# Kernel optimization log

Hardware: AMD Instinct MI355X
Metric: run time of the kernel (lower is better)

Reference implementation:

```python
import jax, jax.numpy as jnp
import numpy as np

NUM_HEADS = 16

def setup_inputs() -> dict:
    key = jax.random.key(0)
    ks = jax.random.split(key, 6)
    B, S, D = 2, 2048, 1024
    scale = 1.0 / np.sqrt(D)
    x = jax.random.normal(ks[0], (B, S, D), dtype=jnp.float32)
    mask = jnp.tril(jnp.ones((S, S), dtype=jnp.int32))[None, None, :, :]  # causal [1,1,S,S]
    Wq = jax.random.normal(ks[1], (D, D), dtype=jnp.float32) * scale
    Wk = jax.random.normal(ks[2], (D, D), dtype=jnp.float32) * scale
    Wv = jax.random.normal(ks[3], (D, D), dtype=jnp.float32) * scale
    Wo = jax.random.normal(ks[4], (D, D), dtype=jnp.float32) * scale
    z = jnp.zeros((D,), dtype=jnp.float32)
    return {"x": x, "mask": mask, "Wq": Wq, "bq": z, "Wk": Wk, "bk": z,
            "Wv": Wv, "bv": z, "Wo": Wo, "bo": z}

def reference(x, mask, Wq, bq, Wk, bk, Wv, bv, Wo, bo):
    B, S, D = x.shape
    H = NUM_HEADS
    hd = D // H
    # torch Linear: y = x @ W.T + b
    def proj(W, b):
        return (x @ W.T + b).reshape(B, S, H, hd).transpose(0, 2, 1, 3)  # [B,H,S,hd]
    q = proj(Wq, bq)
    k = proj(Wk, bk)
    v = proj(Wv, bv)
    # NOTE: original module does NOT scale by 1/sqrt(d_k) -- faithful to source.
    scores = jnp.einsum('bhqd,bhkd->bhqk', q, k)  # [B,H,S,S]
    scores = jnp.where(mask == 0, jnp.float32(-10000.0), scores)
    attn = jax.nn.softmax(scores, axis=-1)
    # dropout omitted for deterministic reference (eval-mode equivalent)
    out = jnp.einsum('bhqk,bhkd->bhqd', attn, v)
    out = out.transpose(0, 2, 1, 3).reshape(B, S, D)
    return out @ Wo.T + bo
```

## Files before the change

### kernel.cpp

```cpp
#include <hip/hip_runtime.h>

#define S_LEN 2048
#define DM    1024
#define NHEAD 16
#define HDIM  64
#define NB    2
#define NROWS (NB * S_LEN)
#define RCP_LN2 1.44269504f

using f32x4  = __attribute__((ext_vector_type(4))) float;
using f16x8  = __attribute__((ext_vector_type(8))) _Float16;
using f16x2  = __attribute__((ext_vector_type(2))) _Float16;

__device__ __forceinline__ ushort f2h(float f) {
  return __builtin_bit_cast(ushort, (_Float16)f);
}
__device__ __forceinline__ unsigned pkrtz(float a, float b) {
  return __builtin_bit_cast(unsigned, __builtin_amdgcn_cvt_pkrtz(a, b));
}
__device__ __forceinline__ f32x4 mfma16(f16x8 a, f16x8 b, f32x4 c) {
  return __builtin_amdgcn_mfma_f32_16x16x32_f16(a, b, c, 0, 0, 0);
}
__device__ __forceinline__ void async16(const ushort* g, ushort* l) {
  __builtin_amdgcn_global_load_lds(
      (const __attribute__((address_space(1))) unsigned*)g,
      (__attribute__((address_space(3))) unsigned*)l, 16, 0, 0);
}

__global__ void tohalf5(const float* __restrict__ x,  const float* __restrict__ wq,
                        const float* __restrict__ wk, const float* __restrict__ wv,
                        const float* __restrict__ wo,
                        ushort* __restrict__ Xh, ushort* __restrict__ Wh,
                        ushort* __restrict__ Woh) {
  constexpr int X4 = (NROWS * DM) / 4;
  constexpr int W4 = (DM * DM) / 4;
  const size_t WN = (size_t)DM * DM;
  int i = blockIdx.x * 256 + threadIdx.x;
  const float4* src; ushort4* dst; int k;
  if (i < X4)               { src = (const float4*)x;  dst = (ushort4*)Xh;        k = i; }
  else if (i < X4 + W4)     { src = (const float4*)wq; dst = (ushort4*)Wh;        k = i - X4; }
  else if (i < X4 + 2*W4)   { src = (const float4*)wk; dst = (ushort4*)(Wh+WN);   k = i - X4 - W4; }
  else if (i < X4 + 3*W4)   { src = (const float4*)wv; dst = (ushort4*)(Wh+2*WN); k = i - X4 - 2*W4; }
  else                      { src = (const float4*)wo; dst = (ushort4*)Woh;       k = i - X4 - 3*W4; }
  float4 v = src[k];
  dst[k] = make_ushort4(f2h(v.x), f2h(v.y), f2h(v.z), f2h(v.w));
}

template<int EPI, int MFRAG, int NFRAG>
__global__ __launch_bounds__(256, 4)
void gemm_half(const ushort* __restrict__ A, const ushort* __restrict__ B,
               const float* __restrict__ biasQ, const float* __restrict__ biasK,
               const float* __restrict__ biasV,
               float* __restrict__ outF,
               ushort* __restrict__ Q, ushort* __restrict__ Kd,
               ushort* __restrict__ Vt, int Ncols)
{
  constexpr int KD = 1024;
  constexpr int BM = MFRAG * 32, BN = NFRAG * 32;
  constexpr int NCH = (BM + BN) / 8;
  constexpr int CPW = NCH / 4;
  __shared__ ushort sL[(BM + BN) * 64];
  const int t = threadIdx.x;
  const int w = t >> 6, l = t & 63;
  const int lr = l >> 4, lc = l & 15;
  const int wr = w >> 1, wc = w & 1;
  const int nwg = gridDim.x * gridDim.y;
  const int lin = blockIdx.y * gridDim.x + blockIdx.x;
  const int per8 = nwg >> 3;
  const int swz = (lin & 7) * per8 + (lin >> 3);
  const int i0 = (swz / gridDim.x) * BM, j0 = (swz % gridDim.x) * BN;

  const int srow = l >> 3;
  const int se   = ((l & 7) ^ srow) << 3;

  f32x4 acc[MFRAG][NFRAG] = {};

  for (int k0 = 0; k0 < KD; k0 += 64) {
#pragma unroll
    for (int ii = 0; ii < CPW; ++ii) {
      const int c = w * CPW + ii;
      const ushort* src = (c < BM / 8)
          ? A + (size_t)(i0 + c * 8 + srow) * KD + k0 + se
          : B + (size_t)(j0 + (c - BM / 8) * 8 + srow) * KD + k0 + se;
      async16(src, &sL[c * 512]);
    }
    asm volatile("s_waitcnt vmcnt(0)" ::: "memory");
    __syncthreads();
#pragma unroll
    for (int kk = 0; kk < 2; ++kk) {
      const int cb = (kk * 64 + lr * 16) ^ ((lc & 7) << 4);
      f16x8 a[MFRAG], b[NFRAG];
#pragma unroll
      for (int m = 0; m < MFRAG; ++m)
        a[m] = *(const f16x8*)&sL[(wr * MFRAG * 16 + m * 16 + lc) * 64 + (cb >> 1)];
#pragma unroll
      for (int n = 0; n < NFRAG; ++n)
        b[n] = *(const f16x8*)&sL[BM * 64 + (wc * NFRAG * 16 + n * 16 + lc) * 64 + (cb >> 1)];
#pragma unroll
      for (int m = 0; m < MFRAG; ++m)
#pragma unroll
        for (int n = 0; n < NFRAG; ++n)
          acc[m][n] = mfma16(a[m], b[n], acc[m][n]);
    }
    __syncthreads();
  }

#pragma unroll
  for (int m = 0; m < MFRAG; ++m)
#pragma unroll
    for (int n = 0; n < NFRAG; ++n) {
      const int jbase = j0 + wc * NFRAG * 16 + n * 16;
      const int ibase = i0 + wr * MFRAG * 16 + m * 16 + lr * 4;
      if constexpr (EPI == 0) {
        const int region = jbase >> 10;
        const int jc0 = jbase & 1023;
        const int h = jc0 >> 6, d0 = jc0 & 63;
        const int b = ibase >> 11, s0 = ibase & 2047;
        const size_t bh = (size_t)(b * NHEAD + h);
        if (region == 0) {
          float bb = biasQ[jc0 + lc];
#pragma unroll
          for (int r = 0; r < 4; ++r)
            Q[(bh * S_LEN + s0 + r) * HDIM + d0 + lc] =
                f2h((acc[m][n][r] + bb) * RCP_LN2);
        } else if (region == 1) {
          float bb = biasK[jc0 + lc];
#pragma unroll
          for (int r = 0; r < 4; ++r)
            Kd[(bh * S_LEN + s0 + r) * HDIM + d0 + lc] = f2h(acc[m][n][r] + bb);
        } else {
          float bb = biasV[jc0 + lc];
          ushort4 pv = make_ushort4(f2h(acc[m][n][0] + bb), f2h(acc[m][n][1] + bb),
                                    f2h(acc[m][n][2] + bb), f2h(acc[m][n][3] + bb));
          *(ushort4*)&Vt[(bh * HDIM + d0 + lc) * S_LEN + s0] = pv;
        }
      } else {
#pragma unroll
        for (int r = 0; r < 4; ++r)
          outF[(size_t)(ibase + r) * Ncols + jbase + lc] =
              acc[m][n][r] + biasQ[jbase + lc];
      }
    }
}

__global__ __launch_bounds__(128, 4)
void attn_kernel(const ushort* __restrict__ Qp, const ushort* __restrict__ Kp,
                 const ushort* __restrict__ Vt, ushort* __restrict__ O)
{
  __shared__ ushort sKV[2 * 64 * 64];
  __shared__ ushort Plds[2][16][72];
  const int lin = blockIdx.x;
  const int v  = 63 - (lin >> 5);
  const int bh = lin & 31;
  const int t = threadIdx.x, w = t >> 6, l = t & 63;
  const int g = l >> 4, q = l & 15;
  const size_t base = (size_t)bh * S_LEN * HDIM;
  const int q0 = v * 32 + w * 16;
  const int nkt = (v >> 1) + 1;

  const int srow = l >> 3;
  const int se   = ((l & 7) ^ srow) << 3;

  f16x8 bQ[2];
#pragma unroll
  for (int ks = 0; ks < 2; ++ks)
    bQ[ks] = *(const f16x8*)(Qp + base + (size_t)(q0 + q) * HDIM + ks * 32 + g * 8);

  f32x4 oacc[4] = {};
  float m = -3e38f, lsum = 0.f;

  for (int kt = 0; kt < nkt; ++kt) {
#pragma unroll
    for (int ii = 0; ii < 8; ++ii) {
      const int c = w * 8 + ii;
      const int sel = c >> 3, sub = c & 7;
      const ushort* src =
          sel == 0 ? Kp + base + (size_t)(kt * 64 + sub * 8 + srow) * HDIM + se
                   : Vt + ((size_t)bh * HDIM + sub * 8 + srow) * S_LEN + kt * 64 + se;
      async16(src, &sKV[sel * 4096 + sub * 512]);
    }
    asm volatile("s_waitcnt vmcnt(0)" ::: "memory");
    __syncthreads();

    f32x4 s[4] = {};
#pragma unroll
    for (int ks = 0; ks < 2; ++ks) {
      const int cb = (((ks * 64 + g * 16) ^ ((q & 7) << 4)) >> 1);
#pragma unroll
      for (int n = 0; n < 4; ++n) {
        f16x8 kf = *(const f16x8*)&sKV[(n * 16 + q) * 64 + cb];
        s[n] = mfma16(kf, bQ[ks], s[n]);
      }
    }
    if (kt == nkt - 1) {
      const int qg = q0 + q;
#pragma unroll
      for (int n = 0; n < 4; ++n)
#pragma unroll
        for (int r = 0; r < 4; ++r) {
          int kg = kt * 64 + n * 16 + g * 4 + r;
          if (kg > qg) s[n][r] = -1e30f;
        }
    }
    float pm = -3e38f;
#pragma unroll
    for (int n = 0; n < 4; ++n) {
      pm = fmaxf(pm, fmaxf(fmaxf(s[n][0], s[n][1]), fmaxf(s[n][2], s[n][3])));
    }
    pm = fmaxf(pm, __shfl_xor(pm, 16));
    pm = fmaxf(pm, __shfl_xor(pm, 32));
    if (__any(pm > m + 8.0f)) {
      float mnew = fmaxf(m, pm);
      float sc = exp2f(m - mnew);
      m = mnew;
      float scr[4];
#pragma unroll
      for (int r = 0; r < 4; ++r) scr[r] = __shfl(sc, g * 4 + r);
#pragma unroll
      for (int dt = 0; dt < 4; ++dt)
#pragma unroll
        for (int r = 0; r < 4; ++r) oacc[dt][r] *= scr[r];
      lsum *= sc;
    }
    float rs = 0.f;
#pragma unroll
    for (int n = 0; n < 4; ++n)
#pragma unroll
      for (int r = 0; r < 4; ++r) {
        float pe = exp2f(s[n][r] - m);
        s[n][r] = pe;
        rs += pe;
      }
    rs += __shfl_xor(rs, 16);
    rs += __shfl_xor(rs, 32);
    lsum += rs;

#pragma unroll
    for (int n = 0; n < 4; ++n) {
      uint2 pk = make_uint2(pkrtz(s[n][0], s[n][1]), pkrtz(s[n][2], s[n][3]));
      *(uint2*)&Plds[w][q][n * 16 + g * 4] = pk;
    }
#pragma unroll
    for (int ks = 0; ks < 2; ++ks) {
      f16x8 ap = *(const f16x8*)&Plds[w][q][ks * 32 + g * 8];
      const int cb = (((ks * 64 + g * 16) ^ ((q & 7) << 4)) >> 1);
#pragma unroll
      for (int dt = 0; dt < 4; ++dt) {
        f16x8 bv = *(const f16x8*)&sKV[4096 + (dt * 16 + q) * 64 + cb];
        oacc[dt] = mfma16(ap, bv, oacc[dt]);
      }
    }
    __syncthreads();
  }

  float lsr[4];
#pragma unroll
  for (int r = 0; r < 4; ++r)
    lsr[r] = __builtin_amdgcn_rcpf(__shfl(lsum, g * 4 + r));
  const int b = bh >> 4, h = bh & 15;
#pragma unroll
  for (int dt = 0; dt < 4; ++dt)
#pragma unroll
    for (int r = 0; r < 4; ++r) {
      int qg = q0 + g * 4 + r;
      O[((size_t)b * S_LEN + qg) * DM + h * HDIM + dt * 16 + q] =
          f2h(oacc[dt][r] * lsr[r]);
    }
}

extern "C" void kernel_launch(void* const* d_in, const int* in_sizes, int n_in,
                              void* d_out, int out_size, void* d_ws, size_t ws_size,
                              hipStream_t stream)
{
  const float* x  = (const float*)d_in[0];
  const float* Wq = (const float*)d_in[2];
  const float* bq = (const float*)d_in[3];
  const float* Wk = (const float*)d_in[4];
  const float* bk = (const float*)d_in[5];
  const float* Wv = (const float*)d_in[6];
  const float* bv = (const float*)d_in[7];
  const float* Wo = (const float*)d_in[8];
  const float* bo = (const float*)d_in[9];
  float* out = (float*)d_out;

  char* ws = (char*)d_ws;
  size_t off = 0;
  auto alloc = [&](size_t bytes) { char* p = ws + off; off += bytes; return p; };
  const size_t XN = (size_t)NROWS * DM;
  const size_t WN = (size_t)DM * DM;

  ushort* Xh  = (ushort*)alloc(XN * 2);
  ushort* Wh  = (ushort*)alloc(3 * WN * 2);
  ushort* Woh = (ushort*)alloc(WN * 2);
  ushort* Qb  = (ushort*)alloc(XN * 2);
  ushort* Kb  = (ushort*)alloc(XN * 2);
  ushort* Vt  = (ushort*)alloc(XN * 2);
  ushort* Ob  = (ushort*)alloc(XN * 2);
  (void)ws_size; (void)in_sizes; (void)n_in; (void)out_size;

  const int total4 = (int)(XN / 4 + 4 * (WN / 4));
  tohalf5<<<total4 / 256, 256, 0, stream>>>(x, Wq, Wk, Wv, Wo, Xh, Wh, Woh);

  gemm_half<0, 4, 4><<<dim3(24, 32), 256, 0, stream>>>(
      Xh, Wh, bq, bk, bv, nullptr, Qb, Kb, Vt, 3072);
  attn_kernel<<<2048, 128, 0, stream>>>(Qb, Kb, Vt, Ob);
  gemm_half<1, 2, 4><<<dim3(8, 64), 256, 0, stream>>>(
      Ob, Woh, bo, nullptr, nullptr, out, nullptr, nullptr, nullptr, 1024);
}
```

Measured before the change: 122.6 us.

## Enlarge attention query tile to 128 rows with double-buffered K/V staging

Each attention block now covers 128 query rows with 4 waves, each wave handling two 16-row sub-tiles, so every K/V tile loaded into LDS is reused by twice as many queries. K/V loads are double-buffered so the next tile is fetched while the current one is computed, and waves skip tiles that lie fully above their causal diagonal. This reduces global K/V traffic and exposed load latency, at the cost of more registers and LDS per block, fewer blocks (512), and possible load imbalance between waves in the causal region.

```diff
diff --git a/kernel.cpp b/kernel.cpp
--- a/kernel.cpp
+++ b/kernel.cpp
@@ -10,7 +10,6 @@
 
 using f32x4  = __attribute__((ext_vector_type(4))) float;
 using f16x8  = __attribute__((ext_vector_type(8))) _Float16;
-using f16x2  = __attribute__((ext_vector_type(2))) _Float16;
 
 __device__ __forceinline__ ushort f2h(float f) {
   return __builtin_bit_cast(ushort, (_Float16)f);
@@ -143,129 +142,165 @@
     }
 }
 
-__global__ __launch_bounds__(128, 4)
+__global__ __launch_bounds__(256, 3)
 void attn_kernel(const ushort* __restrict__ Qp, const ushort* __restrict__ Kp,
                  const ushort* __restrict__ Vt, ushort* __restrict__ O)
 {
-  __shared__ ushort sKV[2 * 64 * 64];
-  __shared__ ushort Plds[2][16][72];
+  __shared__ ushort sKV[2][2 * 64 * 64];
+  __shared__ ushort Plds[4][2][16][72];
   const int lin = blockIdx.x;
-  const int v  = 63 - (lin >> 5);
+  const int qi = 15 - (lin >> 5);
   const int bh = lin & 31;
   const int t = threadIdx.x, w = t >> 6, l = t & 63;
   const int g = l >> 4, q = l & 15;
   const size_t base = (size_t)bh * S_LEN * HDIM;
-  const int q0 = v * 32 + w * 16;
-  const int nkt = (v >> 1) + 1;
+  const int q0w = qi * 128 + w * 32;
+  const int nkt = 2 * qi + 2;
 
   const int srow = l >> 3;
   const int se   = ((l & 7) ^ srow) << 3;
 
-  f16x8 bQ[2];
-#pragma unroll
-  for (int ks = 0; ks < 2; ++ks)
-    bQ[ks] = *(const f16x8*)(Qp + base + (size_t)(q0 + q) * HDIM + ks * 32 + g * 8);
-
-  f32x4 oacc[4] = {};
-  float m = -3e38f, lsum = 0.f;
+  auto stage = [&](int buf, int kt) {
+#pragma unroll
+    for (int ii = 0; ii < 4; ++ii) {
+      const int c = w * 4 + ii;
+      const int sel = c >> 3, sub = c & 7;
+      const ushort* src = sel == 0
+          ? Kp + base + (size_t)(kt * 64 + sub * 8 + srow) * HDIM + se
+          : Vt + ((size_t)bh * HDIM + sub * 8 + srow) * S_LEN + kt * 64 + se;
+      async16(src, &sKV[buf][sel * 4096 + sub * 512]);
+    }
+  };
+
+  f16x8 bQ[2][2];
+#pragma unroll
+  for (int u = 0; u < 2; ++u)
+#pragma unroll
+    for (int ks = 0; ks < 2; ++ks)
+      bQ[u][ks] = *(const f16x8*)(Qp + base +
+                  (size_t)(q0w + u * 16 + q) * HDIM + ks * 32 + g * 8);
+
+  f32x4 oacc[2][4] = {};
+  float m[2] = {-3e38f, -3e38f}, lsum[2] = {0.f, 0.f};
+
+  stage(0, 0);
+  asm volatile("s_waitcnt vmcnt(0)" ::: "memory");
+  __syncthreads();
+  int cur = 0;
 
   for (int kt = 0; kt < nkt; ++kt) {
-#pragma unroll
-    for (int ii = 0; ii < 8; ++ii) {
-      const int c = w * 8 + ii;
-      const int sel = c >> 3, sub = c & 7;
-      const ushort* src =
-          sel == 0 ? Kp + base + (size_t)(kt * 64 + sub * 8 + srow) * HDIM + se
-                   : Vt + ((size_t)bh * HDIM + sub * 8 + srow) * S_LEN + kt * 64 + se;
-      async16(src, &sKV[sel * 4096 + sub * 512]);
+    if (kt + 1 < nkt) stage(cur ^ 1, kt + 1);
+
+    if (kt * 64 <= q0w + 31) {
+      f32x4 s[2][4] = {};
+#pragma unroll
+      for (int ks = 0; ks < 2; ++ks) {
+        const int cb = (((ks * 64 + g * 16) ^ ((q & 7) << 4)) >> 1);
+#pragma unroll
+        for (int n = 0; n < 4; ++n) {
+          f16x8 kf = *(const f16x8*)&sKV[cur][(n * 16 + q) * 64 + cb];
+          s[0][n] = mfma16(kf, bQ[0][ks], s[0][n]);
+          s[1][n] = mfma16(kf, bQ[1][ks], s[1][n]);
+        }
+      }
+#pragma unroll
+      for (int u = 0; u < 2; ++u) {
+        if (kt * 64 + 63 > q0w + u * 16) {
+          const int qg = q0w + u * 16 + q;
+#pragma unroll
+          for (int n = 0; n < 4; ++n)
+#pragma unroll
+            for (int r = 0; r < 4; ++r) {
+              int kg = kt * 64 + n * 16 + g * 4 + r;
+              if (kg > qg) s[u][n][r] = -1e30f;
+            }
+        }
+      }
+      float pm[2];
+#pragma unroll
+      for (int u = 0; u < 2; ++u) {
+        float p = -3e38f;
+#pragma unroll
+        for (int n = 0; n < 4; ++n)
+          p = fmaxf(p, fmaxf(fmaxf(s[u][n][0], s[u][n][1]),
+                             fmaxf(s[u][n][2], s[u][n][3])));
+        p = fmaxf(p, __shfl_xor(p, 16));
+        p = fmaxf(p, __shfl_xor(p, 32));
+        pm[u] = p;
+      }
+#pragma unroll
+      for (int u = 0; u < 2; ++u) {
+        if (__any(pm[u] > m[u] + 8.0f)) {
+          float mnew = fmaxf(m[u], pm[u]);
+          float sc = exp2f(m[u] - mnew);
+          m[u] = mnew;
+          float scr[4];
+#pragma unroll
+          for (int r = 0; r < 4; ++r) scr[r] = __shfl(sc, g * 4 + r);
+#pragma unroll
+          for (int dt = 0; dt < 4; ++dt)
+#pragma unroll
+            for (int r = 0; r < 4; ++r) oacc[u][dt][r] *= scr[r];
+          lsum[u] *= sc;
+        }
+      }
+#pragma unroll
+      for (int u = 0; u < 2; ++u) {
+        float rs = 0.f;
+#pragma unroll
+        for (int n = 0; n < 4; ++n)
+#pragma unroll
+          for (int r = 0; r < 4; ++r) {
+            float pe = exp2f(s[u][n][r] - m[u]);
+            s[u][n][r] = pe;
+            rs += pe;
+          }
+        rs += __shfl_xor(rs, 16);
+        rs += __shfl_xor(rs, 32);
+        lsum[u] += rs;
+      }
+#pragma unroll
+      for (int u = 0; u < 2; ++u)
+#pragma unroll
+        for (int n = 0; n < 4; ++n) {
+          uint2 pk = make_uint2(pkrtz(s[u][n][0], s[u][n][1]),
+                                pkrtz(s[u][n][2], s[u][n][3]));
+          *(uint2*)&Plds[w][u][q][n * 16 + g * 4] = pk;
+        }
+#pragma unroll
+      for (int ks = 0; ks < 2; ++ks) {
+        const int cb = (((ks * 64 + g * 16) ^ ((q & 7) << 4)) >> 1);
+        f16x8 ap0 = *(const f16x8*)&Plds[w][0][q][ks * 32 + g * 8];
+        f16x8 ap1 = *(const f16x8*)&Plds[w][1][q][ks * 32 + g * 8];
+#pragma unroll
+        for (int dt = 0; dt < 4; ++dt) {
+          f16x8 bv = *(const f16x8*)&sKV[cur][4096 + (dt * 16 + q) * 64 + cb];
+          oacc[0][dt] = mfma16(ap0, bv, oacc[0][dt]);
+          oacc[1][dt] = mfma16(ap1, bv, oacc[1][dt]);
+        }
+      }
     }
     asm volatile("s_waitcnt vmcnt(0)" ::: "memory");
     __syncthreads();
-
-    f32x4 s[4] = {};
-#pragma unroll
-    for (int ks = 0; ks < 2; ++ks) {
-      const int cb = (((ks * 64 + g * 16) ^ ((q & 7) << 4)) >> 1);
-#pragma unroll
-      for (int n = 0; n < 4; ++n) {
-        f16x8 kf = *(const f16x8*)&sKV[(n * 16 + q) * 64 + cb];
-        s[n] = mfma16(kf, bQ[ks], s[n]);
-      }
-    }
-    if (kt == nkt - 1) {
-      const int qg = q0 + q;
-#pragma unroll
-      for (int n = 0; n < 4; ++n)
-#pragma unroll
-        for (int r = 0; r < 4; ++r) {
-          int kg = kt * 64 + n * 16 + g * 4 + r;
-          if (kg > qg) s[n][r] = -1e30f;
-        }
-    }
-    float pm = -3e38f;
-#pragma unroll
-    for (int n = 0; n < 4; ++n) {
-      pm = fmaxf(pm, fmaxf(fmaxf(s[n][0], s[n][1]), fmaxf(s[n][2], s[n][3])));
-    }
-    pm = fmaxf(pm, __shfl_xor(pm, 16));
-    pm = fmaxf(pm, __shfl_xor(pm, 32));
-    if (__any(pm > m + 8.0f)) {
-      float mnew = fmaxf(m, pm);
-      float sc = exp2f(m - mnew);
-      m = mnew;
-      float scr[4];
-#pragma unroll
-      for (int r = 0; r < 4; ++r) scr[r] = __shfl(sc, g * 4 + r);
-#pragma unroll
-      for (int dt = 0; dt < 4; ++dt)
-#pragma unroll
-        for (int r = 0; r < 4; ++r) oacc[dt][r] *= scr[r];
-      lsum *= sc;
-    }
-    float rs = 0.f;
-#pragma unroll
-    for (int n = 0; n < 4; ++n)
+    cur ^= 1;
+  }
+
+  const int b = bh >> 4, h = bh & 15;
+#pragma unroll
+  for (int u = 0; u < 2; ++u) {
+    float lsr[4];
+#pragma unroll
+    for (int r = 0; r < 4; ++r)
+      lsr[r] = __builtin_amdgcn_rcpf(__shfl(lsum[u], g * 4 + r));
+#pragma unroll
+    for (int dt = 0; dt < 4; ++dt)
 #pragma unroll
       for (int r = 0; r < 4; ++r) {
-        float pe = exp2f(s[n][r] - m);
-        s[n][r] = pe;
-        rs += pe;
-      }
-    rs += __shfl_xor(rs, 16);
-    rs += __shfl_xor(rs, 32);
-    lsum += rs;
-
-#pragma unroll
-    for (int n = 0; n < 4; ++n) {
-      uint2 pk = make_uint2(pkrtz(s[n][0], s[n][1]), pkrtz(s[n][2], s[n][3]));
-      *(uint2*)&Plds[w][q][n * 16 + g * 4] = pk;
-    }
-#pragma unroll
-    for (int ks = 0; ks < 2; ++ks) {
-      f16x8 ap = *(const f16x8*)&Plds[w][q][ks * 32 + g * 8];
-      const int cb = (((ks * 64 + g * 16) ^ ((q & 7) << 4)) >> 1);
-#pragma unroll
-      for (int dt = 0; dt < 4; ++dt) {
-        f16x8 bv = *(const f16x8*)&sKV[4096 + (dt * 16 + q) * 64 + cb];
-        oacc[dt] = mfma16(ap, bv, oacc[dt]);
-      }
-    }
-    __syncthreads();
+        int qg = q0w + u * 16 + g * 4 + r;
+        O[((size_t)b * S_LEN + qg) * DM + h * HDIM + dt * 16 + q] =
+            f2h(oacc[u][dt][r] * lsr[r]);
+      }
   }
-
-  float lsr[4];
-#pragma unroll
-  for (int r = 0; r < 4; ++r)
-    lsr[r] = __builtin_amdgcn_rcpf(__shfl(lsum, g * 4 + r));
-  const int b = bh >> 4, h = bh & 15;
-#pragma unroll
-  for (int dt = 0; dt < 4; ++dt)
-#pragma unroll
-    for (int r = 0; r < 4; ++r) {
-      int qg = q0 + g * 4 + r;
-      O[((size_t)b * S_LEN + qg) * DM + h * HDIM + dt * 16 + q] =
-          f2h(oacc[dt][r] * lsr[r]);
-    }
 }
 
 extern "C" void kernel_launch(void* const* d_in, const int* in_sizes, int n_in,
@@ -303,7 +338,7 @@
 
   gemm_half<0, 4, 4><<<dim3(24, 32), 256, 0, stream>>>(
       Xh, Wh, bq, bk, bv, nullptr, Qb, Kb, Vt, 3072);
-  attn_kernel<<<2048, 128, 0, stream>>>(Qb, Kb, Vt, Ob);
+  attn_kernel<<<512, 256, 0, stream>>>(Qb, Kb, Vt, Ob);
   gemm_half<1, 2, 4><<<dim3(8, 64), 256, 0, stream>>>(
       Ob, Woh, bo, nullptr, nullptr, out, nullptr, nullptr, nullptr, 1024);
 }
```

Result: slower. 128.5 us (+4.8%).
